# Kernel optimization log

Measured on AMD Instinct MI355X. Metric: run time of the kernel, lower is better.

## Reference

```python
import jax, jax.numpy as jnp
import numpy as np

B, C, H, W = 32, 256, 64, 64
MH = 8
E = 524288
TEMPERATURE = 0.1
LN_EPS = 1e-5


def setup_inputs() -> dict:
    key = jax.random.key(0)
    ks = jax.random.split(key, 6)
    n_nodes = B * H * W
    scale = 1.0 / np.sqrt(C).astype(np.float32)
    img = jax.random.normal(ks[0], (B, C, H, W), jnp.float32)
    all_edge = jax.random.randint(ks[1], (2, E), 0, n_nodes, dtype=jnp.int64)
    Wp = jax.random.normal(ks[2], (C, C), jnp.float32) * scale
    bp = jnp.zeros((C,), jnp.float32)
    Wg = jax.random.normal(ks[3], (C, C), jnp.float32) * scale
    bg = jnp.zeros((C,), jnp.float32)
    ln_gamma = jnp.ones((C,), jnp.float32)
    ln_beta = jnp.zeros((C,), jnp.float32)
    diff_query = jax.random.normal(ks[4], (1, 1, C), jnp.float32) * scale  # xavier-ish
    return {"img": img, "all_edge": all_edge, "Wp": Wp, "bp": bp,
            "Wg": Wg, "bg": bg, "ln_gamma": ln_gamma, "ln_beta": ln_beta,
            "diff_query": diff_query, "mask_head": MH}


def _gcn_conv(x, row, col, Wg, bg, num_nodes):
    # PyG GCNConv with add_self_loops=True, symmetric normalization.
    loop = jnp.arange(num_nodes, dtype=row.dtype)
    row = jnp.concatenate([row, loop])
    col = jnp.concatenate([col, loop])
    deg = jnp.zeros((num_nodes,), x.dtype).at[col].add(1.0)
    dinv = jnp.where(deg > 0, jax.lax.rsqrt(deg), 0.0)
    norm = dinv[row] * dinv[col]                      # [E+N]
    xl = x @ Wg                                       # [N, C]
    msg = xl[row] * norm[:, None]                     # gather + scale
    agg = jax.ops.segment_sum(msg, col, num_segments=num_nodes)
    return agg + bg


def reference(img, all_edge, Wp, bp, Wg, bg, ln_gamma, ln_beta, diff_query, mask_head):
    b, c, h, w = img.shape
    node_num = h * w
    num_nodes = b * node_num
    hd = c // mask_head
    # [B,C,H,W] -> [B, N, C]
    x = jnp.transpose(img, (0, 2, 3, 1)).reshape(b, node_num, c)
    x = x @ Wp + bp
    x = x.reshape(num_nodes, c)
    g = _gcn_conv(x, all_edge[0], all_edge[1], Wg, bg, num_nodes)
    g = jax.nn.gelu(g, approximate=False)             # nn.GELU (exact)
    g = g + x
    mu = jnp.mean(g, axis=-1, keepdims=True)
    var = jnp.mean(jnp.square(g - mu), axis=-1, keepdims=True)
    img_graph = (g - mu) * jax.lax.rsqrt(var + LN_EPS) * ln_gamma + ln_beta
    # multi-head adjacency: query [B*MH, 1, hd], keys [B*MH, N, hd]
    q = jnp.broadcast_to(diff_query, (b, 1, c)).reshape(b * mask_head, 1, hd)
    k = img_graph.reshape(b, node_num, mask_head, hd)
    k = jnp.transpose(k, (0, 2, 1, 3)).reshape(b * mask_head, node_num, hd)
    adj = jnp.einsum('bod,bnd->bon', q, k) / TEMPERATURE
    adj = jax.nn.softmax(adj, axis=-1)
    return img_graph, adj
```

## Files before the change

### kernel.cpp

```cpp
#include <hip/hip_runtime.h>
#include <hip/hip_bf16.h>

typedef unsigned short u16;
typedef __attribute__((ext_vector_type(8))) short short8;
typedef __attribute__((ext_vector_type(16))) float f32x16;

#define AS1C(p) ((const __attribute__((address_space(1))) void*)(p))
#define AS3(p)  ((__attribute__((address_space(3))) void*)(p))

constexpr int CC    = 256;
constexpr int HWSZ  = 4096;
constexpr int NNODE = 131072;
constexpr int EEDG  = 524288;
constexpr int CAP   = 32;

__device__ __forceinline__ float bf2f(u16 h){ unsigned u = ((unsigned)h)<<16; float f; __builtin_memcpy(&f,&u,4); return f; }
__device__ __forceinline__ u16 f2bf(float f){ unsigned u; __builtin_memcpy(&u,&f,4); return (u16)((u + 0x7FFFu + ((u>>16)&1u))>>16); }

__device__ __forceinline__ unsigned pkbf(float a, float b){
  float2 t; t.x = a; t.y = b;
  __hip_bfloat162 h = __float22bfloat162_rn(t);
  unsigned u; __builtin_memcpy(&u,&h,4); return u;
}

__device__ __forceinline__ float gelu_fast(float v){
  float y = 0.7978845608f*(v + 0.044715f*v*v*v);
  float e = __expf(2.0f*y);
  float r = __builtin_amdgcn_rcpf(e + 1.0f);
  return 0.5f*v*(2.0f - 2.0f*r);
}

__device__ __forceinline__ void unpack8(uint4 q, float f[8]){
  unsigned w0=q.x,w1=q.y,w2=q.z,w3=q.w;
  unsigned l0=w0<<16, h0=w0&0xffff0000u, l1=w1<<16, h1=w1&0xffff0000u;
  unsigned l2=w2<<16, h2=w2&0xffff0000u, l3=w3<<16, h3=w3&0xffff0000u;
  __builtin_memcpy(&f[0],&l0,4); __builtin_memcpy(&f[1],&h0,4);
  __builtin_memcpy(&f[2],&l1,4); __builtin_memcpy(&f[3],&h1,4);
  __builtin_memcpy(&f[4],&l2,4); __builtin_memcpy(&f[5],&h2,4);
  __builtin_memcpy(&f[6],&l3,4); __builtin_memcpy(&f[7],&h3,4);
}

__global__ __launch_bounds__(256) void transpose_split(const float* __restrict__ src,
                                                       u16* __restrict__ dhi, u16* __restrict__ dlo,
                                                       int R, int Ccols, size_t sb_in, size_t sb_out)
{
  __shared__ float t[64][65];
  const float* s = src + blockIdx.z*sb_in + (size_t)(blockIdx.y*64)*Ccols + blockIdx.x*64;
  size_t obase   = blockIdx.z*sb_out + (size_t)(blockIdx.x*64)*R + blockIdx.y*64;
  int tid = threadIdx.x;
  for (int i=0;i<4;++i){
    int idx = i*256 + tid;
    int r = idx>>4, q = idx&15;
    float4 v = *(const float4*)(s + (size_t)r*Ccols + q*4);
    t[r][q*4+0]=v.x; t[r][q*4+1]=v.y; t[r][q*4+2]=v.z; t[r][q*4+3]=v.w;
  }
  __syncthreads();
  for (int i=0;i<2;++i){
    int idx = i*256 + tid;
    int rr = idx>>3, ch = idx&7;
    u16 hi[8], lo[8];
    for (int j=0;j<8;++j){
      float f = t[ch*8+j][rr];
      u16 h = f2bf(f); hi[j] = h;
      lo[j] = f2bf(f - bf2f(h));
    }
    *(uint4*)(dhi + obase + (size_t)rr*R + ch*8) = *(uint4*)hi;
    if (dlo) *(uint4*)(dlo + obase + (size_t)rr*R + ch*8) = *(uint4*)lo;
  }
}

__global__ __launch_bounds__(256,3) void gemm_t1(const float* __restrict__ img,
                                                 const u16* __restrict__ Bt,
                                                 const float* __restrict__ bias,
                                                 u16* __restrict__ C)
{
  __shared__ u16 As[2][64*32];
  __shared__ u16 Bs[2][256*32];
  const int tid = threadIdx.x, wid = tid>>6, lane = tid&63;
  const int row0 = blockIdx.x*64;
  const int bb = row0>>12, hw0 = row0&4095;
  const float* abase = img + (size_t)bb*CC*HWSZ + hw0;
  const int l31 = lane&31, lh = lane>>5;
  const int mpr = l31;
  const int cb  = wid*8 + lh*4;
  const int cs  = wid ^ (mpr&3);
  const int wa0 = (2*mpr  )*32 + cs*8 + lh*4;
  const int wa1 = (2*mpr+1)*32 + cs*8 + lh*4;

  f32x16 acc[2][2];
  #pragma unroll
  for (int i=0;i<2;++i)
    #pragma unroll
    for (int j=0;j<2;++j)
      #pragma unroll
      for (int e=0;e<16;++e) acc[i][j][e]=0.f;

  float2 arX[4], arY[4];

#define LOADA(dst, kt)                                                                 \
  { _Pragma("unroll")                                                                  \
    for (int i=0;i<4;++i)                                                              \
      dst[i] = *(const float2*)(abase + (size_t)((kt)+cb+i)*HWSZ + 2*mpr); }

#define WRITEA(buf, src)                                                               \
  { uint2 p0, p1;                                                                      \
    p0.x = pkbf(src[0].x, src[1].x); p0.y = pkbf(src[2].x, src[3].x);                  \
    p1.x = pkbf(src[0].y, src[1].y); p1.y = pkbf(src[2].y, src[3].y);                  \
    *(uint2*)&As[buf][wa0] = p0;                                                       \
    *(uint2*)&As[buf][wa1] = p1; }

#define STAGE_B(buf, kt)                                                               \
  { _Pragma("unroll")                                                                  \
    for (int it=0; it<4; ++it){                                                        \
      int qb = (it*4+wid)*64;                                                          \
      int q  = qb + lane;                                                              \
      int m  = q>>2, sc = q&3;                                                         \
      int gs = sc ^ ((m>>1)&3);                                                        \
      __builtin_amdgcn_global_load_lds(AS1C(Bt + (size_t)m*256 + (kt) + gs*8),         \
                                       AS3(&Bs[buf][qb*8]), 16, 0, 0); } }

#define STEP(t, XR, YR)                                                                \
  { const int cur = (t)&1;                                                             \
    if ((t) < 7) STAGE_B(cur^1, ((t)+1)*32)                                            \
    if ((t) < 6) LOADA(YR, ((t)+2)*32)                                                 \
    short8 af[2][2], bfr[2][2];                                                        \
    _Pragma("unroll")                                                                  \
    for (int fm=0; fm<2; ++fm)                                                         \
      _Pragma("unroll")                                                                \
      for (int kh=0; kh<2; ++kh) {                                                     \
        int row = fm*32 + l31;                                                         \
        int sa  = (kh*2 + lh) ^ ((row>>1)&3);                                          \
        af[fm][kh] = *(const short8*)&As[cur][row*32 + sa*8];                          \
      }                                                                                \
    _Pragma("unroll")                                                                  \
    for (int fn=0; fn<2; ++fn)                                                         \
      _Pragma("unroll")                                                                \
      for (int kh=0; kh<2; ++kh) {                                                     \
        int col = wid*64 + fn*32 + l31;                                                \
        int sb  = (kh*2 + lh) ^ ((col>>1)&3);                                          \
        bfr[fn][kh] = *(const short8*)&Bs[cur][col*32 + sb*8];                         \
      }                                                                                \
    _Pragma("unroll")                                                                  \
    for (int kh=0; kh<2; ++kh)                                                         \
      _Pragma("unroll")                                                                \
      for (int fm=0; fm<2; ++fm)                                                       \
        _Pragma("unroll")                                                              \
        for (int fn=0; fn<2; ++fn)                                                     \
          acc[fm][fn] = __builtin_amdgcn_mfma_f32_32x32x16_bf16(af[fm][kh], bfr[fn][kh], acc[fm][fn], 0, 0, 0); \
    if ((t) < 7) {                                                                     \
      WRITEA(cur^1, XR)                                                                \
      if ((t) < 6) { asm volatile("s_waitcnt vmcnt(8) lgkmcnt(0)" ::: "memory"); }     \
      else         { asm volatile("s_waitcnt vmcnt(0) lgkmcnt(0)" ::: "memory"); }     \
      __builtin_amdgcn_s_barrier();                                                    \
      __builtin_amdgcn_sched_barrier(0);                                               \
    } }

  LOADA(arX, 0)
  STAGE_B(0, 0)
  asm volatile("s_waitcnt vmcnt(4)" ::: "memory");
  WRITEA(0, arX)
  LOADA(arX, 32)
  asm volatile("s_waitcnt vmcnt(8) lgkmcnt(0)" ::: "memory");
  __builtin_amdgcn_s_barrier();
  __builtin_amdgcn_sched_barrier(0);

  for (int tt=0; tt<8; tt+=2) {
    STEP(tt,   arX, arY)
    STEP(tt+1, arY, arX)
  }
#undef STEP
#undef STAGE_B
#undef WRITEA
#undef LOADA

  #pragma unroll
  for (int fn=0; fn<2; ++fn) {
    int col = wid*64 + fn*32 + l31;
    float bv = bias ? bias[col] : 0.f;
    #pragma unroll
    for (int fm=0; fm<2; ++fm) {
      int rbase = row0 + fm*32 + 4*lh;
      #pragma unroll
      for (int reg=0; reg<16; ++reg) {
        int row = rbase + (reg&3) + 8*(reg>>2);
        C[(size_t)row*256 + col] = f2bf(acc[fm][fn][reg] + bv);
      }
    }
  }
}

__global__ __launch_bounds__(256,3) void gemm1p(const u16* __restrict__ A,
                                                const u16* __restrict__ Bt,
                                                const float* __restrict__ bias,
                                                u16* __restrict__ C)
{
  __shared__ u16 As[2][64*32];
  __shared__ u16 Bs[2][256*32];
  const int tid = threadIdx.x, wid = tid>>6, lane = tid&63;
  const int row0 = blockIdx.x*64;
  const int l31 = lane&31, lh = lane>>5;

  f32x16 acc[2][2];
  #pragma unroll
  for (int i=0;i<2;++i)
    #pragma unroll
    for (int j=0;j<2;++j)
      #pragma unroll
      for (int e=0;e<16;++e) acc[i][j][e]=0.f;

#define STAGE_AB(buf, kt)                                                              \
  {                                                                                    \
    {                                                                                  \
      int qb = wid*64;                                                                 \
      int q  = qb + lane;                                                              \
      int m  = q>>2, sc = q&3;                                                         \
      int gs = sc ^ ((m>>1)&3);                                                        \
      __builtin_amdgcn_global_load_lds(AS1C(A + (size_t)(row0+m)*256 + (kt) + gs*8),   \
                                       AS3(&As[buf][qb*8]), 16, 0, 0);                 \
    }                                                                                  \
    _Pragma("unroll")                                                                  \
    for (int it=0; it<4; ++it){                                                        \
      int qb = (it*4+wid)*64;                                                          \
      int q  = qb + lane;                                                              \
      int m  = q>>2, sc = q&3;                                                         \
      int gs = sc ^ ((m>>1)&3);                                                        \
      __builtin_amdgcn_global_load_lds(AS1C(Bt + (size_t)m*256 + (kt) + gs*8),         \
                                       AS3(&Bs[buf][qb*8]), 16, 0, 0);                 \
    }                                                                                  \
  }

  STAGE_AB(0, 0)
  asm volatile("s_waitcnt vmcnt(0)" ::: "memory");
  __syncthreads();

  for (int t=0; t<8; ++t) {
    int cur = t&1;
    if (t<7) STAGE_AB(cur^1, (t+1)*32)

    short8 af[2][2], bfr[2][2];
    #pragma unroll
    for (int fm=0; fm<2; ++fm)
      #pragma unroll
      for (int kh=0; kh<2; ++kh) {
        int row = fm*32 + l31;
        int sa  = (kh*2 + lh) ^ ((row>>1)&3);
        af[fm][kh] = *(const short8*)&As[cur][row*32 + sa*8];
      }
    #pragma unroll
    for (int fn=0; fn<2; ++fn)
      #pragma unroll
      for (int kh=0; kh<2; ++kh) {
        int col = wid*64 + fn*32 + l31;
        int sb  = (kh*2 + lh) ^ ((col>>1)&3);
        bfr[fn][kh] = *(const short8*)&Bs[cur][col*32 + sb*8];
      }
    #pragma unroll
    for (int kh=0; kh<2; ++kh)
      #pragma unroll
      for (int fm=0; fm<2; ++fm)
        #pragma unroll
        for (int fn=0; fn<2; ++fn)
          acc[fm][fn] = __builtin_amdgcn_mfma_f32_32x32x16_bf16(af[fm][kh], bfr[fn][kh], acc[fm][fn], 0, 0, 0);
    asm volatile("s_waitcnt vmcnt(0)" ::: "memory");
    __syncthreads();
  }
#undef STAGE_AB

  #pragma unroll
  for (int fn=0; fn<2; ++fn) {
    int col = wid*64 + fn*32 + l31;
    float bv = bias ? bias[col] : 0.f;
    #pragma unroll
    for (int fm=0; fm<2; ++fm) {
      int rbase = row0 + fm*32 + 4*lh;
      #pragma unroll
      for (int reg=0; reg<16; ++reg) {
        int row = rbase + (reg&3) + 8*(reg>>2);
        C[(size_t)row*256 + col] = f2bf(acc[fm][fn][reg] + bv);
      }
    }
  }
}

__global__ void fill_all(const int* __restrict__ row, const int* __restrict__ col,
                         int* __restrict__ cur, int* __restrict__ bucket){
  int e = blockIdx.x*256 + threadIdx.x;
  if (e >= EEDG) return;
  int c = col[e];
  int s = atomicAdd(&cur[c], 1);
  if (s < CAP) bucket[(size_t)c*CAP + s] = row[e];
}
__global__ void calc_dinv(const int* __restrict__ cnt, float* __restrict__ dinv){
  int n = blockIdx.x*256 + threadIdx.x;
  if (n < NNODE) dinv[n] = rsqrtf((float)cnt[n] + 1.0f);
}

__global__ __launch_bounds__(256) void fused_agg(
    const u16* __restrict__ xl, const u16* __restrict__ xhi,
    const int* __restrict__ cnt, const float* __restrict__ dinv, const int* __restrict__ bucket,
    const float* __restrict__ bgv, const float* __restrict__ gam, const float* __restrict__ bet,
    const float* __restrict__ qv, float* __restrict__ outg, float* __restrict__ logits)
{
  const int wid = threadIdx.x>>6, lane = threadIdx.x&63;
  const int half = lane>>5, sl = lane&31;
  const int n = blockIdx.x*8 + wid*2 + half;
  const int c0 = sl*8;
  const float dn = dinv[n];
  int lim = cnt[n]; if (lim > CAP) lim = CAP;

  int rl = bucket[(size_t)n*CAP + sl];
  if (sl >= lim) rl = n;
  float wl = (sl < lim) ? dinv[rl]*dn : 0.0f;

  uint4 qh = *(const uint4*)(xhi + (size_t)n*256 + c0);

  float a[8];
  {
    uint4 q = *(const uint4*)(xl + (size_t)n*256 + c0);
    unpack8(q, a);
    float wself = dn*dn;
    #pragma unroll
    for (int j=0;j<8;++j) a[j] *= wself;
  }

  int limR = (lim + 3) & ~3;
  for (int s=0; s<limR; s+=4) {
    int b0 = half*32 + s;
    int  r0 = __shfl(rl, b0),   r1 = __shfl(rl, b0+1);
    int  r2 = __shfl(rl, b0+2), r3 = __shfl(rl, b0+3);
    float w0 = __shfl(wl, b0),   w1 = __shfl(wl, b0+1);
    float w2 = __shfl(wl, b0+2), w3 = __shfl(wl, b0+3);
    uint4 q0 = *(const uint4*)(xl + (size_t)r0*256 + c0);
    uint4 q1 = *(const uint4*)(xl + (size_t)r1*256 + c0);
    uint4 q2 = *(const uint4*)(xl + (size_t)r2*256 + c0);
    uint4 q3 = *(const uint4*)(xl + (size_t)r3*256 + c0);
    float f0[8], f1[8], f2[8], f3[8];
    unpack8(q0, f0); unpack8(q1, f1); unpack8(q2, f2); unpack8(q3, f3);
    #pragma unroll
    for (int j=0;j<8;++j) a[j] += f0[j]*w0 + f1[j]*w1 + f2[j]*w2 + f3[j]*w3;
  }

  float xv[8];
  unpack8(qh, xv);

  float4 b0v = *(const float4*)(bgv + c0), b1v = *(const float4*)(bgv + c0 + 4);
  float bgs[8] = {b0v.x,b0v.y,b0v.z,b0v.w,b1v.x,b1v.y,b1v.z,b1v.w};
  float g[8];
  float s1 = 0.f, s2 = 0.f;
  #pragma unroll
  for (int j=0;j<8;++j){
    g[j] = gelu_fast(a[j] + bgs[j]) + xv[j];
    s1 += g[j]; s2 += g[j]*g[j];
  }
  #pragma unroll
  for (int off=16; off; off>>=1){ s1 += __shfl_xor(s1, off); s2 += __shfl_xor(s2, off); }
  float mu  = s1*(1.0f/256.0f);
  float var = s2*(1.0f/256.0f) - mu*mu;
  float inv = rsqrtf(var + 1e-5f);

  float4 g0 = *(const float4*)(gam + c0), g1 = *(const float4*)(gam + c0 + 4);
  float4 e0 = *(const float4*)(bet + c0), e1 = *(const float4*)(bet + c0 + 4);
  float gms[8] = {g0.x,g0.y,g0.z,g0.w,g1.x,g1.y,g1.z,g1.w};
  float bts[8] = {e0.x,e0.y,e0.z,e0.w,e1.x,e1.y,e1.z,e1.w};
  float y[8];
  #pragma unroll
  for (int j=0;j<8;++j) y[j] = (g[j]-mu)*inv*gms[j] + bts[j];

  float4 o0 = {y[0],y[1],y[2],y[3]}, o1 = {y[4],y[5],y[6],y[7]};
  *reinterpret_cast<float4*>(outg + (size_t)n*256 + c0)     = o0;
  *reinterpret_cast<float4*>(outg + (size_t)n*256 + c0 + 4) = o1;

  float4 q0 = *(const float4*)(qv + c0), q1 = *(const float4*)(qv + c0 + 4);
  float qs[8] = {q0.x,q0.y,q0.z,q0.w,q1.x,q1.y,q1.z,q1.w};
  float dq = 0.f;
  #pragma unroll
  for (int j=0;j<8;++j) dq += y[j]*qs[j];
  dq += __shfl_xor(dq,1); dq += __shfl_xor(dq,2);
  if ((sl&3)==0){
    int b = n>>12, p = n&4095, h = sl>>2;
    logits[(size_t)(b*8+h)*4096 + p] = dq*10.0f;
  }
}

__global__ __launch_bounds__(256) void softmax_rows(const float* __restrict__ logits, float* __restrict__ outa){
  int r = blockIdx.x;
  const float* p = logits + (size_t)r*4096;
  int tid = threadIdx.x;
  int wid = tid>>6, lane = tid&63;
  __shared__ float redm[4];
  __shared__ float reds[4];
  float v[16];
  float mx = -1e30f;
  for (int i=0;i<16;++i){ v[i] = p[tid + i*256]; mx = fmaxf(mx, v[i]); }
  for (int off=32; off; off>>=1) mx = fmaxf(mx, __shfl_xor(mx, off));
  if (lane==0) redm[wid]=mx;
  __syncthreads();
  mx = fmaxf(fmaxf(redm[0],redm[1]), fmaxf(redm[2],redm[3]));
  float sum = 0.f;
  for (int i=0;i<16;++i){ v[i] = expf(v[i]-mx); sum += v[i]; }
  for (int off=32; off; off>>=1) sum += __shfl_xor(sum, off);
  if (lane==0) reds[wid]=sum;
  __syncthreads();
  sum = reds[0]+reds[1]+reds[2]+reds[3];
  float rinv = 1.0f/sum;
  for (int i=0;i<16;++i) outa[(size_t)r*4096 + tid + i*256] = v[i]*rinv;
}

extern "C" void kernel_launch(void* const* d_in, const int* in_sizes, int n_in,
                              void* d_out, int out_size, void* d_ws, size_t ws_size,
                              hipStream_t stream)
{
  const float* img  = (const float*)d_in[0];
  const int* edges  = (const int*)d_in[1];
  const float* Wp   = (const float*)d_in[2];
  const float* bp   = (const float*)d_in[3];
  const float* Wg   = (const float*)d_in[4];
  const float* bg   = (const float*)d_in[5];
  const float* lng  = (const float*)d_in[6];
  const float* lnb  = (const float*)d_in[7];
  const float* dq   = (const float*)d_in[8];
  char* ws = (char*)d_ws;

  constexpr size_t REG  = (size_t)NNODE*CC*2;
  constexpr size_t WTS  = 2u*131072;
  constexpr size_t GBLK = 524288u*2 + (size_t)NNODE*CAP*4 + (size_t)256*4096*4;
  if (ws_size < 2*REG + WTS + GBLK) return;

  u16* buf0 = (u16*)(ws + 0);
  u16* buf1 = (u16*)(ws + REG);
  char* wts  = ws + 2*REG;
  char* gblk = wts + WTS;

  u16* WpT_hi = (u16*)(wts);
  u16* WgT_hi = (u16*)(wts + 131072);
  int*   cur    = (int*)(gblk);
  float* dinv   = (float*)(gblk + 524288);
  int*   bucket = (int*)(gblk + 1048576);
  float* logits = (float*)(gblk + 1048576 + (size_t)NNODE*CAP*4);

  transpose_split<<<dim3(4,4,1), 256, 0, stream>>>(Wp, WpT_hi, nullptr, 256, 256, 0, 0);
  transpose_split<<<dim3(4,4,1), 256, 0, stream>>>(Wg, WgT_hi, nullptr, 256, 256, 0, 0);

  hipMemsetAsync(cur, 0, 524288, stream);
  fill_all <<<2048, 256, 0, stream>>>(edges, edges+EEDG, cur, bucket);
  calc_dinv<<<512,  256, 0, stream>>>(cur, dinv);

  gemm_t1<<<2048, 256, 0, stream>>>(img, WpT_hi, bp, buf0);
  gemm1p<<<2048, 256, 0, stream>>>(buf0, WgT_hi, nullptr, buf1);

  float* outg = (float*)d_out;
  float* outa = (float*)d_out + (size_t)NNODE*CC;
  fused_agg<<<NNODE/8, 256, 0, stream>>>(buf1, buf0, cur, dinv, bucket,
                                         bg, lng, lnb, dq, outg, logits);
  softmax_rows<<<256, 256, 0, stream>>>(logits, outa);
}
```

Measured before the change: 230.1 us.

## Raise GEMM occupancy, swizzle block order, tighten waitcnt, widen gather unroll

Raises the launch-bounds occupancy hint from 3 to 4 waves per SIMD on both GEMM kernels and remaps block indices with a stride-8 swizzle in the image-transposing GEMM. It also tightens the vmcnt wait from 8 to 4 outstanding loads in that GEMM's pipeline. In the GCN aggregation, the neighbor gather is unrolled from 4 to 8 rows per iteration for more memory-level parallelism. The aim is better latency hiding, at the risk of register spills in the GEMMs, stalls from the tighter wait, and wasted padded loads when neighbor counts are small.

```diff
diff --git a/kernel.cpp b/kernel.cpp
--- a/kernel.cpp
+++ b/kernel.cpp
@@ -69,7 +69,7 @@
   }
 }
 
-__global__ __launch_bounds__(256,3) void gemm_t1(const float* __restrict__ img,
+__global__ __launch_bounds__(256,4) void gemm_t1(const float* __restrict__ img,
                                                  const u16* __restrict__ Bt,
                                                  const float* __restrict__ bias,
                                                  u16* __restrict__ C)
@@ -77,7 +77,8 @@
   __shared__ u16 As[2][64*32];
   __shared__ u16 Bs[2][256*32];
   const int tid = threadIdx.x, wid = tid>>6, lane = tid&63;
-  const int row0 = blockIdx.x*64;
+  const int bxs = (blockIdx.x & 7)*256 + (blockIdx.x >> 3);
+  const int row0 = bxs*64;
   const int bb = row0>>12, hw0 = row0&4095;
   const float* abase = img + (size_t)bb*CC*HWSZ + hw0;
   const int l31 = lane&31, lh = lane>>5;
@@ -149,7 +150,7 @@
           acc[fm][fn] = __builtin_amdgcn_mfma_f32_32x32x16_bf16(af[fm][kh], bfr[fn][kh], acc[fm][fn], 0, 0, 0); \
     if ((t) < 7) {                                                                     \
       WRITEA(cur^1, XR)                                                                \
-      if ((t) < 6) { asm volatile("s_waitcnt vmcnt(8) lgkmcnt(0)" ::: "memory"); }     \
+      if ((t) < 6) { asm volatile("s_waitcnt vmcnt(4) lgkmcnt(0)" ::: "memory"); }     \
       else         { asm volatile("s_waitcnt vmcnt(0) lgkmcnt(0)" ::: "memory"); }     \
       __builtin_amdgcn_s_barrier();                                                    \
       __builtin_amdgcn_sched_barrier(0);                                               \
@@ -160,7 +161,7 @@
   asm volatile("s_waitcnt vmcnt(4)" ::: "memory");
   WRITEA(0, arX)
   LOADA(arX, 32)
-  asm volatile("s_waitcnt vmcnt(8) lgkmcnt(0)" ::: "memory");
+  asm volatile("s_waitcnt vmcnt(4) lgkmcnt(0)" ::: "memory");
   __builtin_amdgcn_s_barrier();
   __builtin_amdgcn_sched_barrier(0);
 
@@ -189,7 +190,7 @@
   }
 }
 
-__global__ __launch_bounds__(256,3) void gemm1p(const u16* __restrict__ A,
+__global__ __launch_bounds__(256,4) void gemm1p(const u16* __restrict__ A,
                                                 const u16* __restrict__ Bt,
                                                 const float* __restrict__ bias,
                                                 u16* __restrict__ C)
@@ -323,21 +324,32 @@
     for (int j=0;j<8;++j) a[j] *= wself;
   }
 
-  int limR = (lim + 3) & ~3;
-  for (int s=0; s<limR; s+=4) {
+  int limR = (lim + 7) & ~7;
+  for (int s=0; s<limR; s+=8) {
     int b0 = half*32 + s;
-    int  r0 = __shfl(rl, b0),   r1 = __shfl(rl, b0+1);
-    int  r2 = __shfl(rl, b0+2), r3 = __shfl(rl, b0+3);
+    int rr0 = __shfl(rl, b0),   rr1 = __shfl(rl, b0+1);
+    int rr2 = __shfl(rl, b0+2), rr3 = __shfl(rl, b0+3);
+    int rr4 = __shfl(rl, b0+4), rr5 = __shfl(rl, b0+5);
+    int rr6 = __shfl(rl, b0+6), rr7 = __shfl(rl, b0+7);
     float w0 = __shfl(wl, b0),   w1 = __shfl(wl, b0+1);
     float w2 = __shfl(wl, b0+2), w3 = __shfl(wl, b0+3);
-    uint4 q0 = *(const uint4*)(xl + (size_t)r0*256 + c0);
-    uint4 q1 = *(const uint4*)(xl + (size_t)r1*256 + c0);
-    uint4 q2 = *(const uint4*)(xl + (size_t)r2*256 + c0);
-    uint4 q3 = *(const uint4*)(xl + (size_t)r3*256 + c0);
-    float f0[8], f1[8], f2[8], f3[8];
+    float w4 = __shfl(wl, b0+4), w5 = __shfl(wl, b0+5);
+    float w6 = __shfl(wl, b0+6), w7 = __shfl(wl, b0+7);
+    uint4 q0 = *(const uint4*)(xl + (size_t)rr0*256 + c0);
+    uint4 q1 = *(const uint4*)(xl + (size_t)rr1*256 + c0);
+    uint4 q2 = *(const uint4*)(xl + (size_t)rr2*256 + c0);
+    uint4 q3 = *(const uint4*)(xl + (size_t)rr3*256 + c0);
+    uint4 q4 = *(const uint4*)(xl + (size_t)rr4*256 + c0);
+    uint4 q5 = *(const uint4*)(xl + (size_t)rr5*256 + c0);
+    uint4 q6 = *(const uint4*)(xl + (size_t)rr6*256 + c0);
+    uint4 q7 = *(const uint4*)(xl + (size_t)rr7*256 + c0);
+    float f0[8], f1[8], f2[8], f3[8], f4[8], f5[8], f6[8], f7[8];
     unpack8(q0, f0); unpack8(q1, f1); unpack8(q2, f2); unpack8(q3, f3);
-    #pragma unroll
-    for (int j=0;j<8;++j) a[j] += f0[j]*w0 + f1[j]*w1 + f2[j]*w2 + f3[j]*w3;
+    unpack8(q4, f4); unpack8(q5, f5); unpack8(q6, f6); unpack8(q7, f7);
+    #pragma unroll
+    for (int j=0;j<8;++j)
+      a[j] += f0[j]*w0 + f1[j]*w1 + f2[j]*w2 + f3[j]*w3
+            + f4[j]*w4 + f5[j]*w5 + f6[j]*w6 + f7[j]*w7;
   }
 
   float xv[8];
```

Result: slower. 241.1 us (+4.8%).
